# Kernel tuning notes

Hardware: AMD Instinct MI355X
Metric: run time of the kernel (lower is better)

The kernel has to match this reference:

```python
import jax, jax.numpy as jnp
import numpy as np

D_MODEL, EMB_DIM, ORDER, SEQ_LEN, BATCH = 768, 33, 64, 8192, 2


def setup_inputs() -> dict:
    key = jax.random.key(0)
    ks = jax.random.split(key, 9)
    x = jax.random.normal(ks[0], (BATCH, D_MODEL, SEQ_LEN), dtype=jnp.float32)

    # PositionalEmbedding: t in [0,1], complex exponential bands
    bands = (EMB_DIM - 1) // 2
    t = jnp.linspace(0.0, 1.0, SEQ_LEN, dtype=jnp.float32)[None, :, None]          # (1, L, 1)
    t_rescaled = jnp.linspace(0.0, SEQ_LEN - 1, SEQ_LEN, dtype=jnp.float32)[None, :, None]
    w_ang = 2.0 * jnp.pi * t_rescaled / SEQ_LEN                                     # (1, L, 1)
    f = jnp.linspace(1e-4, bands - 1, bands, dtype=jnp.float32)[None, None]         # (1, 1, bands)
    zc = jnp.exp(-1j * f.astype(jnp.complex64) * w_ang.astype(jnp.complex64))
    z = jnp.concatenate([t, zc.real, zc.imag], axis=-1)                             # (1, L, emb_dim)

    # Sin activation frequency (shared single instance across all MLP layers), w=1
    freq = jnp.ones((1, ORDER), dtype=jnp.float32)

    def lin(k, fan_out, fan_in):
        s = 1.0 / np.sqrt(fan_in)
        return jax.random.normal(k, (fan_out, fan_in), dtype=jnp.float32) * s

    W1 = lin(ks[1], ORDER, EMB_DIM)
    b1 = jax.random.normal(ks[2], (ORDER,), dtype=jnp.float32) * 0.02
    W2 = lin(ks[3], ORDER, ORDER)
    b2 = jax.random.normal(ks[4], (ORDER,), dtype=jnp.float32) * 0.02
    W3 = lin(ks[5], ORDER, ORDER)
    b3 = jax.random.normal(ks[6], (ORDER,), dtype=jnp.float32) * 0.02
    Wout = lin(ks[7], D_MODEL, ORDER)  # no bias

    # ExponentialModulation deltas (deterministic buffer)
    target, fast_pct, slow_pct = 0.01, 0.3, 1.5
    max_decay = np.log(target) / fast_pct
    min_decay = np.log(target) / slow_pct
    deltas = jnp.linspace(min_decay, max_decay, D_MODEL, dtype=jnp.float32)[None, None]  # (1,1,d)

    bias_D = jax.random.normal(ks[8], (D_MODEL,), dtype=jnp.float32)

    return {"x": x, "L": SEQ_LEN, "z": z, "t": t, "freq": freq,
            "W1": W1, "b1": b1, "W2": W2, "b2": b2, "W3": W3, "b3": b3,
            "Wout": Wout, "deltas": deltas, "bias_D": bias_D}


def reference(x, L, z, t, freq, W1, b1, W2, b2, W3, b3, Wout, deltas, bias_D):
    zL, tL = z[:, :L], t[:, :L]                      # (1, L, emb_dim), (1, L, 1)
    # Implicit filter MLP with shared Sin activation
    h = jnp.sin(freq * (jnp.einsum('ble,oe->blo', zL, W1) + b1))
    h = jnp.sin(freq * (jnp.einsum('blo,po->blp', h, W2) + b2))
    h = jnp.sin(freq * (jnp.einsum('blo,po->blp', h, W3) + b3))
    h = jnp.einsum('blo,do->bld', h, Wout)           # (1, L, d_model)
    # Exponential modulation
    h = h * jnp.exp(-tL * jnp.abs(deltas))
    k = h[0].T                                       # (d_model, L)
    # FFT-based long convolution (fftconv_ref with gelu=False).
    # torch: k_f = rfft(k, n)/n ; y = irfft(u_f*k_f, n, norm='forward') == standard irfft(u_f*rfft(k,n), n)
    fft_size = 2 * L
    k_f = jnp.fft.rfft(k, n=fft_size)                # (d_model, n//2+1) complex
    u_f = jnp.fft.rfft(x, n=fft_size)                # (B, d_model, n//2+1)
    y = jnp.fft.irfft(u_f * k_f, n=fft_size)[..., :L]
    out = y + x * bias_D[:, None]
    return out.astype(x.dtype)
```

## Files before the change

### kernel.cpp

```cpp
#include <hip/hip_runtime.h>
#include <hip/hip_fp16.h>
#include <math.h>

#define D_MODEL 768
#define EMB 33
#define ORDER 64
#define SEQ 8192
#define BATCH 2
#define M 8192

#define PI_F 3.14159265358979323846f

#define IDX(a) ((a) + ((a) >> 4) + ((a) >> 7))
#define LDS_SZ 8768

__device__ __forceinline__ int rev13(int x) { return (int)(__brev((unsigned)x) >> 19); }

__device__ __constant__ float C8[8] = {
    1.f, 0.9238795325f, 0.7071067812f, 0.3826834324f,
    0.f, -0.3826834324f, -0.7071067812f, -0.9238795325f };
__device__ __constant__ float S8n[8] = {
    0.f, -0.3826834324f, -0.7071067812f, -0.9238795325f,
    -1.f, -0.9238795325f, -0.7071067812f, -0.3826834324f };
__device__ __constant__ float S8p[8] = {
    0.f, 0.3826834324f, 0.7071067812f, 0.9238795325f,
    1.f, 0.9238795325f, 0.7071067812f, 0.3826834324f };

__global__ __launch_bounds__(256) void mlp_kernel(
    const float* __restrict__ z, const float* __restrict__ freq,
    const float* __restrict__ W1, const float* __restrict__ b1,
    const float* __restrict__ W2, const float* __restrict__ b2,
    const float* __restrict__ W3, const float* __restrict__ b3,
    float* __restrict__ h3T)
{
    __shared__ float zt[33 * 72];
    __shared__ float h1[64 * 72];
    __shared__ float h2[64 * 72];
    __shared__ float Wb[64 * 68];
    __shared__ float sfr[64], sb[64];
    int t = threadIdx.x;
    int l0 = blockIdx.x * 64;

    for (int i = t; i < 64 * 33; i += 256) {
        int l = i / 33, e = i - l * 33;
        zt[e * 72 + l] = z[(size_t)(l0 + l) * 33 + e];
    }
    for (int i = t; i < 64 * 33; i += 256) {
        int o = i / 33, e = i - o * 33;
        Wb[e * 68 + o] = W1[i];
    }
    if (t < 64) { sfr[t] = freq[t]; sb[t] = b1[t]; }
    __syncthreads();

    int lx = t & 15, oy = t >> 4;
    float fr4[4], bi4[4], acc[4][4];
#pragma unroll
    for (int i = 0; i < 4; ++i) { fr4[i] = sfr[4 * oy + i]; bi4[i] = sb[4 * oy + i]; }
#pragma unroll
    for (int c = 0; c < 4; ++c)
#pragma unroll
        for (int i = 0; i < 4; ++i) acc[c][i] = bi4[i];
    for (int e = 0; e < 33; ++e) {
        float4 hv = *(const float4*)&zt[e * 72 + 4 * lx];
        float4 wv = *(const float4*)&Wb[e * 68 + 4 * oy];
        float h[4] = {hv.x, hv.y, hv.z, hv.w}, w[4] = {wv.x, wv.y, wv.z, wv.w};
#pragma unroll
        for (int c = 0; c < 4; ++c)
#pragma unroll
            for (int i = 0; i < 4; ++i) acc[c][i] = fmaf(h[c], w[i], acc[c][i]);
    }
#pragma unroll
    for (int i = 0; i < 4; ++i) {
        float4 v = make_float4(__sinf(fr4[i] * acc[0][i]), __sinf(fr4[i] * acc[1][i]),
                               __sinf(fr4[i] * acc[2][i]), __sinf(fr4[i] * acc[3][i]));
        *(float4*)&h1[(4 * oy + i) * 72 + 4 * lx] = v;
    }
    __syncthreads();

    for (int i = t; i < 4096; i += 256) {
        int o = i >> 6, q = i & 63;
        Wb[q * 68 + o] = W2[i];
    }
    if (t < 64) sb[t] = b2[t];
    __syncthreads();
#pragma unroll
    for (int i = 0; i < 4; ++i) bi4[i] = sb[4 * oy + i];
#pragma unroll
    for (int c = 0; c < 4; ++c)
#pragma unroll
        for (int i = 0; i < 4; ++i) acc[c][i] = bi4[i];
    for (int q = 0; q < 64; ++q) {
        float4 hv = *(const float4*)&h1[q * 72 + 4 * lx];
        float4 wv = *(const float4*)&Wb[q * 68 + 4 * oy];
        float h[4] = {hv.x, hv.y, hv.z, hv.w}, w[4] = {wv.x, wv.y, wv.z, wv.w};
#pragma unroll
        for (int c = 0; c < 4; ++c)
#pragma unroll
            for (int i = 0; i < 4; ++i) acc[c][i] = fmaf(h[c], w[i], acc[c][i]);
    }
#pragma unroll
    for (int i = 0; i < 4; ++i) {
        float4 v = make_float4(__sinf(fr4[i] * acc[0][i]), __sinf(fr4[i] * acc[1][i]),
                               __sinf(fr4[i] * acc[2][i]), __sinf(fr4[i] * acc[3][i]));
        *(float4*)&h2[(4 * oy + i) * 72 + 4 * lx] = v;
    }
    __syncthreads();

    for (int i = t; i < 4096; i += 256) {
        int o = i >> 6, q = i & 63;
        Wb[q * 68 + o] = W3[i];
    }
    if (t < 64) sb[t] = b3[t];
    __syncthreads();
#pragma unroll
    for (int i = 0; i < 4; ++i) bi4[i] = sb[4 * oy + i];
#pragma unroll
    for (int c = 0; c < 4; ++c)
#pragma unroll
        for (int i = 0; i < 4; ++i) acc[c][i] = bi4[i];
    for (int q = 0; q < 64; ++q) {
        float4 hv = *(const float4*)&h2[q * 72 + 4 * lx];
        float4 wv = *(const float4*)&Wb[q * 68 + 4 * oy];
        float h[4] = {hv.x, hv.y, hv.z, hv.w}, w[4] = {wv.x, wv.y, wv.z, wv.w};
#pragma unroll
        for (int c = 0; c < 4; ++c)
#pragma unroll
            for (int i = 0; i < 4; ++i) acc[c][i] = fmaf(h[c], w[i], acc[c][i]);
    }
#pragma unroll
    for (int i = 0; i < 4; ++i) {
        float4 v = make_float4(__sinf(fr4[i] * acc[0][i]), __sinf(fr4[i] * acc[1][i]),
                               __sinf(fr4[i] * acc[2][i]), __sinf(fr4[i] * acc[3][i]));
        *(float4*)&h3T[(size_t)(4 * oy + i) * SEQ + l0 + 4 * lx] = v;
    }
}

__global__ __launch_bounds__(256) void filt_kernel(
    const float* __restrict__ h3T, const float* __restrict__ Wout,
    const float* __restrict__ tvec, const float* __restrict__ deltas,
    float* __restrict__ kout)
{
    __shared__ float ht[64 * 132];
    __shared__ float wt[64 * 68];
    int t = threadIdx.x;
    int l0 = blockIdx.x * 128, d0 = blockIdx.y * 64;

    for (int i = t; i < 64 * 128; i += 256) {
        int o = i >> 7, l = i & 127;
        ht[o * 132 + l] = h3T[(size_t)o * SEQ + l0 + l];
    }
    for (int i = t; i < 4096; i += 256) {
        int dd = i >> 6, kk = i & 63;
        wt[kk * 68 + dd] = Wout[(size_t)(d0 + dd) * 64 + kk];
    }
    __syncthreads();

    int lx = t & 31, dy = t >> 5;
    float acc[4][8];
#pragma unroll
    for (int c = 0; c < 4; ++c)
#pragma unroll
        for (int i = 0; i < 8; ++i) acc[c][i] = 0.f;
    for (int kk = 0; kk < 64; ++kk) {
        float4 hv = *(const float4*)&ht[kk * 132 + 4 * lx];
        float4 w0 = *(const float4*)&wt[kk * 68 + 8 * dy];
        float4 w1 = *(const float4*)&wt[kk * 68 + 8 * dy + 4];
        float h[4] = {hv.x, hv.y, hv.z, hv.w};
        float w[8] = {w0.x, w0.y, w0.z, w0.w, w1.x, w1.y, w1.z, w1.w};
#pragma unroll
        for (int c = 0; c < 4; ++c)
#pragma unroll
            for (int i = 0; i < 8; ++i) acc[c][i] = fmaf(h[c], w[i], acc[c][i]);
    }

    float4 tl4 = *(const float4*)&tvec[l0 + 4 * lx];
    float tl[4] = {tl4.x, tl4.y, tl4.z, tl4.w};
    float del[8];
#pragma unroll
    for (int i = 0; i < 8; ++i) del[i] = fabsf(deltas[d0 + 8 * dy + i]);
#pragma unroll
    for (int i = 0; i < 8; ++i) {
        int d = d0 + 8 * dy + i;
        float4 v = make_float4(acc[0][i] * __expf(-tl[0] * del[i]),
                               acc[1][i] * __expf(-tl[1] * del[i]),
                               acc[2][i] * __expf(-tl[2] * del[i]),
                               acc[3][i] * __expf(-tl[3] * del[i]));
        *(float4*)&kout[(size_t)d * SEQ + l0 + 4 * lx] = v;
    }
}

template<int H>
__device__ __forceinline__ void fwd8(float2* A, int t)
{
    constexpr int H4 = H / 4;
    int j0 = t & (H4 - 1);
    float c1, s1;
    __sincosf((-PI_F / (float)H) * (float)j0, &s1, &c1);
#pragma unroll
    for (int gg = 0; gg < 2; ++gg) {
        int g = t + (gg << 9);
        int j = g & (H4 - 1);
        int i = ((g & ~(H4 - 1)) << 3) | j;
        float c1g = c1, s1g = s1;
        if (H4 > 512 && gg == 1) {
            const float cR = 0.9238795325f, sR = -0.3826834324f;
            c1g = c1 * cR - s1 * sR;
            s1g = s1 * cR + c1 * sR;
        }
        float c2 = c1g * c1g - s1g * s1g, s2 = 2.f * c1g * s1g;
        float c3 = c2 * c2 - s2 * s2,     s3 = 2.f * c2 * s2;
        float xr[8], xi[8];
        int ad[8];
#pragma unroll
        for (int m = 0; m < 8; ++m) {
            ad[m] = IDX(i + m * H4);
            float2 v = A[ad[m]];
            xr[m] = v.x; xi[m] = v.y;
        }
        const float r = 0.70710678118f;
        float twc[4], tws[4];
        twc[0] = c1g;             tws[0] = s1g;
        twc[1] = r * (c1g + s1g); tws[1] = r * (s1g - c1g);
        twc[2] = s1g;             tws[2] = -c1g;
        twc[3] = r * (s1g - c1g); tws[3] = -r * (c1g + s1g);
#pragma unroll
        for (int m = 0; m < 4; ++m) {
            float ur = xr[m] + xr[m + 4], ui = xi[m] + xi[m + 4];
            float dr = xr[m] - xr[m + 4], di = xi[m] - xi[m + 4];
            xr[m] = ur; xi[m] = ui;
            xr[m + 4] = dr * twc[m] - di * tws[m];
            xi[m + 4] = dr * tws[m] + di * twc[m];
        }
#pragma unroll
        for (int base = 0; base < 8; base += 4)
#pragma unroll
            for (int mm = 0; mm < 2; ++mm) {
                int a = base + mm, b = a + 2;
                float ur = xr[a] + xr[b], ui = xi[a] + xi[b];
                float dr = xr[a] - xr[b], di = xi[a] - xi[b];
                xr[a] = ur; xi[a] = ui;
                if (mm == 0) { xr[b] = dr * c2 - di * s2; xi[b] = dr * s2 + di * c2; }
                else         { xr[b] = dr * s2 + di * c2; xi[b] = di * s2 - dr * c2; }
            }
#pragma unroll
        for (int m = 0; m < 8; m += 2) {
            float ur = xr[m] + xr[m + 1], ui = xi[m] + xi[m + 1];
            float dr = xr[m] - xr[m + 1], di = xi[m] - xi[m + 1];
            xr[m] = ur; xi[m] = ui;
            xr[m + 1] = dr * c3 - di * s3; xi[m + 1] = dr * s3 + di * c3;
        }
#pragma unroll
        for (int m = 0; m < 8; ++m) A[ad[m]] = make_float2(xr[m], xi[m]);
    }
}

template<int H>
__device__ __forceinline__ void inv8(float2* A, int t)
{
    int j0 = t & (H - 1);
    float ct, st;
    __sincosf((PI_F / (float)(4 * H)) * (float)j0, &st, &ct);
#pragma unroll
    for (int gg = 0; gg < 2; ++gg) {
        int g = t + (gg << 9);
        int j = g & (H - 1);
        int i = ((g & ~(H - 1)) << 3) | j;
        float c = ct, s = st;
        if (H > 512 && gg == 1) {
            const float cR = 0.9238795325f, sR = 0.3826834324f;
            c = ct * cR - st * sR;
            s = st * cR + ct * sR;
        }
        float c2 = c * c - s * s, s2 = 2.f * c * s;
        float c4 = c2 * c2 - s2 * s2, s4 = 2.f * c2 * s2;
        float xr[8], xi[8]; int ad[8];
#pragma unroll
        for (int m = 0; m < 8; ++m) {
            ad[m] = IDX(i + m * H);
            float2 v = A[ad[m]];
            xr[m] = v.x; xi[m] = v.y;
        }
#pragma unroll
        for (int m = 0; m < 8; m += 2) {
            float tr = xr[m + 1] * c4 - xi[m + 1] * s4;
            float ti = xr[m + 1] * s4 + xi[m + 1] * c4;
            xr[m + 1] = xr[m] - tr; xi[m + 1] = xi[m] - ti;
            xr[m]     = xr[m] + tr; xi[m]     = xi[m] + ti;
        }
#pragma unroll
        for (int base = 0; base < 8; base += 4)
#pragma unroll
            for (int mm = 0; mm < 2; ++mm) {
                int a = base + mm, b = a + 2;
                float tr, ti;
                if (mm == 0) { tr = xr[b] * c2 - xi[b] * s2; ti = xr[b] * s2 + xi[b] * c2; }
                else         { tr = -(xr[b] * s2 + xi[b] * c2); ti = xr[b] * c2 - xi[b] * s2; }
                xr[b] = xr[a] - tr; xi[b] = xi[a] - ti;
                xr[a] = xr[a] + tr; xi[a] = xi[a] + ti;
            }
        const float r = 0.70710678118f;
        float t3c[4], t3s[4];
        t3c[0] = c;           t3s[0] = s;
        t3c[1] = r * (c - s); t3s[1] = r * (c + s);
        t3c[2] = -s;          t3s[2] = c;
        t3c[3] = -r * (c + s); t3s[3] = r * (c - s);
#pragma unroll
        for (int m = 0; m < 4; ++m) {
            float tr = xr[m + 4] * t3c[m] - xi[m + 4] * t3s[m];
            float ti = xr[m + 4] * t3s[m] + xi[m + 4] * t3c[m];
            xr[m + 4] = xr[m] - tr; xi[m + 4] = xi[m] - ti;
            xr[m]     = xr[m] + tr; xi[m]     = xi[m] + ti;
        }
#pragma unroll
        for (int m = 0; m < 8; ++m) A[ad[m]] = make_float2(xr[m], xi[m]);
    }
}

__device__ __forceinline__ void fft_fwd(float2* A, int t)
{
    fwd8<4096>(A, t); __syncthreads();
    fwd8<512>(A, t);  __syncthreads();
    fwd8<64>(A, t);   __syncthreads();
    {
        int pb = IDX(16 * t);
        float fr[16], fi[16];
#pragma unroll
        for (int e = 0; e < 16; ++e) { float2 v = A[pb + e]; fr[e] = v.x; fi[e] = v.y; }
#pragma unroll
        for (int k = 0; k < 8; ++k) {
            float cs = C8[k], sn = S8n[k];
            float arr = fr[k], aii = fi[k], brr = fr[k + 8], bii = fi[k + 8];
            fr[k] = arr + brr; fi[k] = aii + bii;
            float dr = arr - brr, di = aii - bii;
            fr[k + 8] = dr * cs - di * sn; fi[k + 8] = dr * sn + di * cs;
        }
#pragma unroll
        for (int b0 = 0; b0 < 16; b0 += 8)
#pragma unroll
            for (int k = 0; k < 4; ++k) {
                float cs = C8[2 * k], sn = S8n[2 * k];
                int i0 = b0 + k, i1 = i0 + 4;
                float arr = fr[i0], aii = fi[i0], brr = fr[i1], bii = fi[i1];
                fr[i0] = arr + brr; fi[i0] = aii + bii;
                float dr = arr - brr, di = aii - bii;
                fr[i1] = dr * cs - di * sn; fi[i1] = dr * sn + di * cs;
            }
#pragma unroll
        for (int b0 = 0; b0 < 16; b0 += 4)
#pragma unroll
            for (int k = 0; k < 2; ++k) {
                float cs = C8[4 * k], sn = S8n[4 * k];
                int i0 = b0 + k, i1 = i0 + 2;
                float arr = fr[i0], aii = fi[i0], brr = fr[i1], bii = fi[i1];
                fr[i0] = arr + brr; fi[i0] = aii + bii;
                float dr = arr - brr, di = aii - bii;
                fr[i1] = dr * cs - di * sn; fi[i1] = dr * sn + di * cs;
            }
#pragma unroll
        for (int b0 = 0; b0 < 16; b0 += 2) {
            float arr = fr[b0], aii = fi[b0], brr = fr[b0 + 1], bii = fi[b0 + 1];
            fr[b0] = arr + brr; fi[b0] = aii + bii;
            fr[b0 + 1] = arr - brr; fi[b0 + 1] = aii - bii;
        }
#pragma unroll
        for (int e = 0; e < 16; ++e) A[pb + e] = make_float2(fr[e], fi[e]);
        __syncthreads();
    }
}

__device__ __forceinline__ void fft_inv(float2* A, int t)
{
    {
        int pb = IDX(16 * t);
        float fr[16], fi[16];
#pragma unroll
        for (int e = 0; e < 16; ++e) { float2 v = A[pb + e]; fr[e] = v.x; fi[e] = v.y; }
#pragma unroll
        for (int b0 = 0; b0 < 16; b0 += 2) {
            float arr = fr[b0], aii = fi[b0], brr = fr[b0 + 1], bii = fi[b0 + 1];
            fr[b0] = arr + brr; fi[b0] = aii + bii;
            fr[b0 + 1] = arr - brr; fi[b0 + 1] = aii - bii;
        }
#pragma unroll
        for (int b0 = 0; b0 < 16; b0 += 4)
#pragma unroll
            for (int k = 0; k < 2; ++k) {
                float cs = C8[4 * k], sn = S8p[4 * k];
                int i0 = b0 + k, i1 = i0 + 2;
                float arr = fr[i0], aii = fi[i0], brr = fr[i1], bii = fi[i1];
                float tr = brr * cs - bii * sn, ti = brr * sn + bii * cs;
                fr[i0] = arr + tr; fi[i0] = aii + ti;
                fr[i1] = arr - tr; fi[i1] = aii - ti;
            }
#pragma unroll
        for (int b0 = 0; b0 < 16; b0 += 8)
#pragma unroll
            for (int k = 0; k < 4; ++k) {
                float cs = C8[2 * k], sn = S8p[2 * k];
                int i0 = b0 + k, i1 = i0 + 4;
                float arr = fr[i0], aii = fi[i0], brr = fr[i1], bii = fi[i1];
                float tr = brr * cs - bii * sn, ti = brr * sn + bii * cs;
                fr[i0] = arr + tr; fi[i0] = aii + ti;
                fr[i1] = arr - tr; fi[i1] = aii - ti;
            }
#pragma unroll
        for (int k = 0; k < 8; ++k) {
            float cs = C8[k], sn = S8p[k];
            float arr = fr[k], aii = fi[k], brr = fr[k + 8], bii = fi[k + 8];
            float tr = brr * cs - bii * sn, ti = brr * sn + bii * cs;
            fr[k] = arr + tr; fi[k] = aii + ti;
            fr[k + 8] = arr - tr; fi[k + 8] = aii - ti;
        }
#pragma unroll
        for (int e = 0; e < 16; ++e) A[pb + e] = make_float2(fr[e], fi[e]);
        __syncthreads();
    }
    inv8<16>(A, t);   __syncthreads();
    inv8<128>(A, t);  __syncthreads();
    inv8<1024>(A, t); __syncthreads();
}

__global__ __launch_bounds__(512, 4) void kf_kernel(float* outk)
{
    __shared__ float2 A[LDS_SZ];
    int t = threadIdx.x, d = blockIdx.x;
    const float* kp = outk + (size_t)d * SEQ;
    for (int n = t; n < 4096; n += 512) {
        A[IDX(n)] = ((const float2*)kp)[n];
    }
    for (int n = 4096 + t; n < M; n += 512) A[IDX(n)] = make_float2(0.f, 0.f);
    __syncthreads();
    fft_fwd(A, t);

    __half2* P0 = (__half2*)(outk + (size_t)d * SEQ);
    __half2* P1 = (__half2*)(outk + (size_t)(D_MODEL + d) * SEQ);
    float cs, sn;
    __sincosf(-PI_F * (float)t * (1.0f / 8192.0f), &sn, &cs);
    const float cRo = 0.9807852804f, sRo = -0.1950903220f;
    for (int j = t; j <= 4096; j += 512) {
        int jm = (M - j) & (M - 1);
        int p0 = rev13(j), p1 = rev13(jm);
        float2 z1 = A[IDX(p0)], z2 = A[IDX(p1)];
        float Ar_ = 0.5f * (z1.x + z2.x), Ai_ = 0.5f * (z1.y - z2.y);
        float Br_ = 0.5f * (z1.y + z2.y), Bi_ = 0.5f * (z2.x - z1.x);
        float wbr = cs * Br_ - sn * Bi_, wbi = cs * Bi_ + sn * Br_;
        float K1r = Ar_ + wbr, K1i = Ai_ + wbi;
        float K2r = Ar_ - wbr, K2i = -(Ai_ - wbi);
        if (j == 0) {
            __half2 v = __floats2half2_rn(K1r, K2r);
            P0[0] = v; P1[0] = v;
        } else {
            __half2 v1 = __floats2half2_rn(K1r, K1i);
            P0[j] = v1; P1[j] = v1;
            if (j != 4096) {
                __half2 v2 = __floats2half2_rn(K2r, K2i);
                P0[M - j] = v2; P1[M - j] = v2;
            }
        }
        float cn = cs * cRo - sn * sRo; sn = sn * cRo + cs * sRo; cs = cn;
    }
}

__global__ __launch_bounds__(512, 4) void conv_kernel(
    const float* __restrict__ x, const float* __restrict__ bias,
    float* outk)
{
    __shared__ float2 A[LDS_SZ];
    int t = threadIdx.x, d = blockIdx.x, b = blockIdx.y;
    const float* xp = x + ((size_t)(b * D_MODEL + d)) * SEQ;
    float bd = bias[d];

#pragma unroll
    for (int idx = 0; idx < 8; ++idx) {
        int n = t + (idx << 9);
        A[IDX(n)] = ((const float2*)xp)[n];
    }
    for (int n = 4096 + t; n < M; n += 512) A[IDX(n)] = make_float2(0.f, 0.f);
    __syncthreads();
    fft_fwd(A, t);

    const __half2* P = (const __half2*)(outk + (size_t)(b * D_MODEL + d) * SEQ);
    float cs, sn;
    __sincosf(-PI_F * (float)t * (1.0f / 8192.0f), &sn, &cs);
    const float cRo = 0.9807852804f, sRo = -0.1950903220f;
    for (int j = t; j <= 4096; j += 512) {
        int jm = (M - j) & (M - 1);
        int p0 = rev13(j), p1 = rev13(jm);
        int q0 = IDX(p0), q1 = IDX(p1);
        float2 z1 = A[q0], z2 = A[q1];
        float Ar_ = 0.5f * (z1.x + z2.x), Ai_ = 0.5f * (z1.y - z2.y);
        float Br_ = 0.5f * (z1.y + z2.y), Bi_ = 0.5f * (z2.x - z1.x);
        float wbr = cs * Br_ - sn * Bi_, wbi = cs * Bi_ + sn * Br_;
        float U1r = Ar_ + wbr, U1i = Ai_ + wbi;
        float U2r = Ar_ - wbr, U2i = -(Ai_ - wbi);
        float K1r, K1i, K2r, K2i;
        if (j == 0) {
            __half2 v = P[0];
            K1r = __low2float(v) + bd;  K1i = 0.f;
            K2r = __high2float(v) + bd; K2i = 0.f;
        } else {
            __half2 v1 = P[j];
            __half2 v2 = P[M - j];
            K1r = __low2float(v1) + bd; K1i = __high2float(v1);
            K2r = __low2float(v2) + bd; K2i = __high2float(v2);
        }
        float P1r = U1r * K1r - U1i * K1i, P1i = U1r * K1i + U1i * K1r;
        float P2r = U2r * K2r - U2i * K2i, P2i = U2r * K2i + U2i * K2r;
        float Er = 0.5f * (P1r + P2r), Ei = 0.5f * (P1i - P2i);
        float Or = 0.5f * (P1r - P2r), Oi = 0.5f * (P1i + P2i);
        float G = cs * Oi - sn * Or;
        float H = cs * Or + sn * Oi;
        A[q0] = make_float2(Er - G, Ei + H);
        if (j != 0) A[q1] = make_float2(Er + G, -Ei + H);
        float cn = cs * cRo - sn * sRo; sn = sn * cRo + cs * sRo; cs = cn;
    }
    __syncthreads();
    fft_inv(A, t);

    const float invM = 1.0f / 8192.0f;
    float* op = outk + ((size_t)(b * D_MODEL + d)) * SEQ;
#pragma unroll
    for (int idx = 0; idx < 8; ++idx) {
        int n = t + (idx << 9);
        float2 v = A[IDX(n)];
        float2 ov;
        ov.x = v.x * invM;
        ov.y = v.y * invM;
        ((float2*)op)[n] = ov;
    }
}

extern "C" void kernel_launch(void* const* d_in, const int* in_sizes, int n_in,
                              void* d_out, int out_size, void* d_ws, size_t ws_size,
                              hipStream_t stream)
{
    (void)in_sizes; (void)n_in; (void)out_size; (void)d_ws; (void)ws_size;
    const float* x      = (const float*)d_in[0];
    const float* z      = (const float*)d_in[2];
    const float* tvec   = (const float*)d_in[3];
    const float* freq   = (const float*)d_in[4];
    const float* W1     = (const float*)d_in[5];
    const float* b1     = (const float*)d_in[6];
    const float* W2     = (const float*)d_in[7];
    const float* b2     = (const float*)d_in[8];
    const float* W3     = (const float*)d_in[9];
    const float* b3     = (const float*)d_in[10];
    const float* Wout   = (const float*)d_in[11];
    const float* deltas = (const float*)d_in[12];
    const float* bias   = (const float*)d_in[13];
    float* out = (float*)d_out;

    float* h3T = out + ((size_t)(2 * D_MODEL - 64) * SEQ);
    float* k   = out;

    hipLaunchKernelGGL(mlp_kernel, dim3(SEQ / 64), dim3(256), 0, stream,
                       z, freq, W1, b1, W2, b2, W3, b3, h3T);
    hipLaunchKernelGGL(filt_kernel, dim3(SEQ / 128, D_MODEL / 64), dim3(256), 0, stream,
                       h3T, Wout, tvec, deltas, k);
    hipLaunchKernelGGL(kf_kernel, dim3(D_MODEL), dim3(512), 0, stream, out);
    hipLaunchKernelGGL(conv_kernel, dim3(D_MODEL, BATCH), dim3(512), 0, stream,
                       x, bias, out);
}
```

Before: 234.1 us.

## Exploit zero padding: split FFT into two half-size transforms with twiddle pre/post

Replaces the full 8192-point complex FFT over a half-zero-padded signal with a first radix-2 stage done analytically at load time. Each input sample is written twice, once plain and once multiplied by a twiddle, so the remaining work is two independent 4096-point FFTs. The inverse is recombined with a twiddle at the store. Blocks now use 1024 threads that each do one radix-8 group per stage, with a radix-8 final stage instead of radix-16. This removes the redundant butterflies on the zero half and the per-thread loop over two groups, at the cost of more threads per block and extra sincos calls in the load and store loops.

```diff
diff --git a/kernel.cpp b/kernel.cpp
--- a/kernel.cpp
+++ b/kernel.cpp
@@ -189,181 +189,149 @@
     }
 }
 
+
+template<int H8>
+__device__ __forceinline__ void fwd8g(float2* A, int t)
+{
+    constexpr int H4 = H8 / 4;
+    int j = t & (H4 - 1);
+    int i = ((t & ~(H4 - 1)) << 3) | j;
+    float c1, s1;
+    __sincosf((-PI_F / (float)H8) * (float)j, &s1, &c1);
+    float c2 = c1 * c1 - s1 * s1, s2 = 2.f * c1 * s1;
+    float c3 = c2 * c2 - s2 * s2, s3 = 2.f * c2 * s2;
+    float xr[8], xi[8];
+    int ad[8];
+#pragma unroll
+    for (int m = 0; m < 8; ++m) {
+        ad[m] = IDX(i + m * H4);
+        float2 v = A[ad[m]];
+        xr[m] = v.x; xi[m] = v.y;
+    }
+    const float r = 0.70710678118f;
+    float twc[4], tws[4];
+    twc[0] = c1;            tws[0] = s1;
+    twc[1] = r * (c1 + s1); tws[1] = r * (s1 - c1);
+    twc[2] = s1;            tws[2] = -c1;
+    twc[3] = r * (s1 - c1); tws[3] = -r * (c1 + s1);
+#pragma unroll
+    for (int m = 0; m < 4; ++m) {
+        float ur = xr[m] + xr[m + 4], ui = xi[m] + xi[m + 4];
+        float dr = xr[m] - xr[m + 4], di = xi[m] - xi[m + 4];
+        xr[m] = ur; xi[m] = ui;
+        xr[m + 4] = dr * twc[m] - di * tws[m];
+        xi[m + 4] = dr * tws[m] + di * twc[m];
+    }
+#pragma unroll
+    for (int base = 0; base < 8; base += 4)
+#pragma unroll
+        for (int mm = 0; mm < 2; ++mm) {
+            int a = base + mm, b = a + 2;
+            float ur = xr[a] + xr[b], ui = xi[a] + xi[b];
+            float dr = xr[a] - xr[b], di = xi[a] - xi[b];
+            xr[a] = ur; xi[a] = ui;
+            if (mm == 0) { xr[b] = dr * c2 - di * s2; xi[b] = dr * s2 + di * c2; }
+            else         { xr[b] = dr * s2 + di * c2; xi[b] = di * s2 - dr * c2; }
+        }
+#pragma unroll
+    for (int m = 0; m < 8; m += 2) {
+        float ur = xr[m] + xr[m + 1], ui = xi[m] + xi[m + 1];
+        float dr = xr[m] - xr[m + 1], di = xi[m] - xi[m + 1];
+        xr[m] = ur; xi[m] = ui;
+        xr[m + 1] = dr * c3 - di * s3; xi[m + 1] = dr * s3 + di * c3;
+    }
+#pragma unroll
+    for (int m = 0; m < 8; ++m) A[ad[m]] = make_float2(xr[m], xi[m]);
+}
+
 template<int H>
-__device__ __forceinline__ void fwd8(float2* A, int t)
-{
-    constexpr int H4 = H / 4;
-    int j0 = t & (H4 - 1);
-    float c1, s1;
-    __sincosf((-PI_F / (float)H) * (float)j0, &s1, &c1);
-#pragma unroll
-    for (int gg = 0; gg < 2; ++gg) {
-        int g = t + (gg << 9);
-        int j = g & (H4 - 1);
-        int i = ((g & ~(H4 - 1)) << 3) | j;
-        float c1g = c1, s1g = s1;
-        if (H4 > 512 && gg == 1) {
-            const float cR = 0.9238795325f, sR = -0.3826834324f;
-            c1g = c1 * cR - s1 * sR;
-            s1g = s1 * cR + c1 * sR;
-        }
-        float c2 = c1g * c1g - s1g * s1g, s2 = 2.f * c1g * s1g;
-        float c3 = c2 * c2 - s2 * s2,     s3 = 2.f * c2 * s2;
-        float xr[8], xi[8];
-        int ad[8];
-#pragma unroll
-        for (int m = 0; m < 8; ++m) {
-            ad[m] = IDX(i + m * H4);
-            float2 v = A[ad[m]];
-            xr[m] = v.x; xi[m] = v.y;
-        }
-        const float r = 0.70710678118f;
-        float twc[4], tws[4];
-        twc[0] = c1g;             tws[0] = s1g;
-        twc[1] = r * (c1g + s1g); tws[1] = r * (s1g - c1g);
-        twc[2] = s1g;             tws[2] = -c1g;
-        twc[3] = r * (s1g - c1g); tws[3] = -r * (c1g + s1g);
-#pragma unroll
-        for (int m = 0; m < 4; ++m) {
-            float ur = xr[m] + xr[m + 4], ui = xi[m] + xi[m + 4];
-            float dr = xr[m] - xr[m + 4], di = xi[m] - xi[m + 4];
-            xr[m] = ur; xi[m] = ui;
-            xr[m + 4] = dr * twc[m] - di * tws[m];
-            xi[m + 4] = dr * tws[m] + di * twc[m];
-        }
-#pragma unroll
-        for (int base = 0; base < 8; base += 4)
-#pragma unroll
-            for (int mm = 0; mm < 2; ++mm) {
-                int a = base + mm, b = a + 2;
-                float ur = xr[a] + xr[b], ui = xi[a] + xi[b];
-                float dr = xr[a] - xr[b], di = xi[a] - xi[b];
-                xr[a] = ur; xi[a] = ui;
-                if (mm == 0) { xr[b] = dr * c2 - di * s2; xi[b] = dr * s2 + di * c2; }
-                else         { xr[b] = dr * s2 + di * c2; xi[b] = di * s2 - dr * c2; }
-            }
-#pragma unroll
-        for (int m = 0; m < 8; m += 2) {
-            float ur = xr[m] + xr[m + 1], ui = xi[m] + xi[m + 1];
-            float dr = xr[m] - xr[m + 1], di = xi[m] - xi[m + 1];
-            xr[m] = ur; xi[m] = ui;
-            xr[m + 1] = dr * c3 - di * s3; xi[m + 1] = dr * s3 + di * c3;
-        }
-#pragma unroll
-        for (int m = 0; m < 8; ++m) A[ad[m]] = make_float2(xr[m], xi[m]);
-    }
-}
-
-template<int H>
-__device__ __forceinline__ void inv8(float2* A, int t)
-{
-    int j0 = t & (H - 1);
-    float ct, st;
-    __sincosf((PI_F / (float)(4 * H)) * (float)j0, &st, &ct);
-#pragma unroll
-    for (int gg = 0; gg < 2; ++gg) {
-        int g = t + (gg << 9);
-        int j = g & (H - 1);
-        int i = ((g & ~(H - 1)) << 3) | j;
-        float c = ct, s = st;
-        if (H > 512 && gg == 1) {
-            const float cR = 0.9238795325f, sR = 0.3826834324f;
-            c = ct * cR - st * sR;
-            s = st * cR + ct * sR;
-        }
-        float c2 = c * c - s * s, s2 = 2.f * c * s;
-        float c4 = c2 * c2 - s2 * s2, s4 = 2.f * c2 * s2;
-        float xr[8], xi[8]; int ad[8];
-#pragma unroll
-        for (int m = 0; m < 8; ++m) {
-            ad[m] = IDX(i + m * H);
-            float2 v = A[ad[m]];
-            xr[m] = v.x; xi[m] = v.y;
-        }
-#pragma unroll
-        for (int m = 0; m < 8; m += 2) {
-            float tr = xr[m + 1] * c4 - xi[m + 1] * s4;
-            float ti = xr[m + 1] * s4 + xi[m + 1] * c4;
-            xr[m + 1] = xr[m] - tr; xi[m + 1] = xi[m] - ti;
-            xr[m]     = xr[m] + tr; xi[m]     = xi[m] + ti;
-        }
-#pragma unroll
-        for (int base = 0; base < 8; base += 4)
-#pragma unroll
-            for (int mm = 0; mm < 2; ++mm) {
-                int a = base + mm, b = a + 2;
-                float tr, ti;
-                if (mm == 0) { tr = xr[b] * c2 - xi[b] * s2; ti = xr[b] * s2 + xi[b] * c2; }
-                else         { tr = -(xr[b] * s2 + xi[b] * c2); ti = xr[b] * c2 - xi[b] * s2; }
-                xr[b] = xr[a] - tr; xi[b] = xi[a] - ti;
-                xr[a] = xr[a] + tr; xi[a] = xi[a] + ti;
-            }
-        const float r = 0.70710678118f;
-        float t3c[4], t3s[4];
-        t3c[0] = c;           t3s[0] = s;
-        t3c[1] = r * (c - s); t3s[1] = r * (c + s);
-        t3c[2] = -s;          t3s[2] = c;
-        t3c[3] = -r * (c + s); t3s[3] = r * (c - s);
-#pragma unroll
-        for (int m = 0; m < 4; ++m) {
-            float tr = xr[m + 4] * t3c[m] - xi[m + 4] * t3s[m];
-            float ti = xr[m + 4] * t3s[m] + xi[m + 4] * t3c[m];
-            xr[m + 4] = xr[m] - tr; xi[m + 4] = xi[m] - ti;
-            xr[m]     = xr[m] + tr; xi[m]     = xi[m] + ti;
-        }
-#pragma unroll
-        for (int m = 0; m < 8; ++m) A[ad[m]] = make_float2(xr[m], xi[m]);
-    }
+__device__ __forceinline__ void inv8g(float2* A, int t)
+{
+    int j = t & (H - 1);
+    int i = ((t & ~(H - 1)) << 3) | j;
+    float c, s;
+    __sincosf((PI_F / (float)(4 * H)) * (float)j, &s, &c);
+    float c2 = c * c - s * s, s2 = 2.f * c * s;
+    float c4 = c2 * c2 - s2 * s2, s4 = 2.f * c2 * s2;
+    float xr[8], xi[8]; int ad[8];
+#pragma unroll
+    for (int m = 0; m < 8; ++m) {
+        ad[m] = IDX(i + m * H);
+        float2 v = A[ad[m]];
+        xr[m] = v.x; xi[m] = v.y;
+    }
+#pragma unroll
+    for (int m = 0; m < 8; m += 2) {
+        float tr = xr[m + 1] * c4 - xi[m + 1] * s4;
+        float ti = xr[m + 1] * s4 + xi[m + 1] * c4;
+        xr[m + 1] = xr[m] - tr; xi[m + 1] = xi[m] - ti;
+        xr[m]     = xr[m] + tr; xi[m]     = xi[m] + ti;
+    }
+#pragma unroll
+    for (int base = 0; base < 8; base += 4)
+#pragma unroll
+        for (int mm = 0; mm < 2; ++mm) {
+            int a = base + mm, b = a + 2;
+            float tr, ti;
+            if (mm == 0) { tr = xr[b] * c2 - xi[b] * s2; ti = xr[b] * s2 + xi[b] * c2; }
+            else         { tr = -(xr[b] * s2 + xi[b] * c2); ti = xr[b] * c2 - xi[b] * s2; }
+            xr[b] = xr[a] - tr; xi[b] = xi[a] - ti;
+            xr[a] = xr[a] + tr; xi[a] = xi[a] + ti;
+        }
+    const float r = 0.70710678118f;
+    float t3c[4], t3s[4];
+    t3c[0] = c;            t3s[0] = s;
+    t3c[1] = r * (c - s);  t3s[1] = r * (c + s);
+    t3c[2] = -s;           t3s[2] = c;
+    t3c[3] = -r * (c + s); t3s[3] = r * (c - s);
+#pragma unroll
+    for (int m = 0; m < 4; ++m) {
+        float tr = xr[m + 4] * t3c[m] - xi[m + 4] * t3s[m];
+        float ti = xr[m + 4] * t3s[m] + xi[m + 4] * t3c[m];
+        xr[m + 4] = xr[m] - tr; xi[m + 4] = xi[m] - ti;
+        xr[m]     = xr[m] + tr; xi[m]     = xi[m] + ti;
+    }
+#pragma unroll
+    for (int m = 0; m < 8; ++m) A[ad[m]] = make_float2(xr[m], xi[m]);
 }
 
 __device__ __forceinline__ void fft_fwd(float2* A, int t)
 {
-    fwd8<4096>(A, t); __syncthreads();
-    fwd8<512>(A, t);  __syncthreads();
-    fwd8<64>(A, t);   __syncthreads();
+    fwd8g<2048>(A, t); __syncthreads();
+    fwd8g<256>(A, t);  __syncthreads();
+    fwd8g<32>(A, t);   __syncthreads();
     {
-        int pb = IDX(16 * t);
-        float fr[16], fi[16];
-#pragma unroll
-        for (int e = 0; e < 16; ++e) { float2 v = A[pb + e]; fr[e] = v.x; fi[e] = v.y; }
-#pragma unroll
-        for (int k = 0; k < 8; ++k) {
-            float cs = C8[k], sn = S8n[k];
-            float arr = fr[k], aii = fi[k], brr = fr[k + 8], bii = fi[k + 8];
-            fr[k] = arr + brr; fi[k] = aii + bii;
-            float dr = arr - brr, di = aii - bii;
-            fr[k + 8] = dr * cs - di * sn; fi[k + 8] = dr * sn + di * cs;
-        }
-#pragma unroll
-        for (int b0 = 0; b0 < 16; b0 += 8)
-#pragma unroll
-            for (int k = 0; k < 4; ++k) {
-                float cs = C8[2 * k], sn = S8n[2 * k];
-                int i0 = b0 + k, i1 = i0 + 4;
-                float arr = fr[i0], aii = fi[i0], brr = fr[i1], bii = fi[i1];
-                fr[i0] = arr + brr; fi[i0] = aii + bii;
-                float dr = arr - brr, di = aii - bii;
-                fr[i1] = dr * cs - di * sn; fi[i1] = dr * sn + di * cs;
-            }
-#pragma unroll
-        for (int b0 = 0; b0 < 16; b0 += 4)
+        int pb = IDX(8 * t);
+        float fr[8], fi[8];
+#pragma unroll
+        for (int e = 0; e < 8; ++e) { float2 v = A[pb + e]; fr[e] = v.x; fi[e] = v.y; }
+#pragma unroll
+        for (int k = 0; k < 4; ++k) {
+            float cs = C8[2 * k], sn = S8n[2 * k];
+            float ar = fr[k], ai = fi[k], br = fr[k + 4], bi = fi[k + 4];
+            fr[k] = ar + br; fi[k] = ai + bi;
+            float dr = ar - br, di = ai - bi;
+            fr[k + 4] = dr * cs - di * sn; fi[k + 4] = dr * sn + di * cs;
+        }
+#pragma unroll
+        for (int b0 = 0; b0 < 8; b0 += 4)
 #pragma unroll
             for (int k = 0; k < 2; ++k) {
                 float cs = C8[4 * k], sn = S8n[4 * k];
                 int i0 = b0 + k, i1 = i0 + 2;
-                float arr = fr[i0], aii = fi[i0], brr = fr[i1], bii = fi[i1];
-                fr[i0] = arr + brr; fi[i0] = aii + bii;
-                float dr = arr - brr, di = aii - bii;
+                float ar = fr[i0], ai = fi[i0], br = fr[i1], bi = fi[i1];
+                fr[i0] = ar + br; fi[i0] = ai + bi;
+                float dr = ar - br, di = ai - bi;
                 fr[i1] = dr * cs - di * sn; fi[i1] = dr * sn + di * cs;
             }
 #pragma unroll
-        for (int b0 = 0; b0 < 16; b0 += 2) {
-            float arr = fr[b0], aii = fi[b0], brr = fr[b0 + 1], bii = fi[b0 + 1];
-            fr[b0] = arr + brr; fi[b0] = aii + bii;
-            fr[b0 + 1] = arr - brr; fi[b0 + 1] = aii - bii;
-        }
-#pragma unroll
-        for (int e = 0; e < 16; ++e) A[pb + e] = make_float2(fr[e], fi[e]);
+        for (int b0 = 0; b0 < 8; b0 += 2) {
+            float ar = fr[b0], ai = fi[b0], br = fr[b0 + 1], bi = fi[b0 + 1];
+            fr[b0] = ar + br; fi[b0] = ai + bi;
+            fr[b0 + 1] = ar - br; fi[b0 + 1] = ai - bi;
+        }
+#pragma unroll
+        for (int e = 0; e < 8; ++e) A[pb + e] = make_float2(fr[e], fi[e]);
         __syncthreads();
     }
 }
@@ -371,64 +339,58 @@
 __device__ __forceinline__ void fft_inv(float2* A, int t)
 {
     {
-        int pb = IDX(16 * t);
-        float fr[16], fi[16];
-#pragma unroll
-        for (int e = 0; e < 16; ++e) { float2 v = A[pb + e]; fr[e] = v.x; fi[e] = v.y; }
-#pragma unroll
-        for (int b0 = 0; b0 < 16; b0 += 2) {
-            float arr = fr[b0], aii = fi[b0], brr = fr[b0 + 1], bii = fi[b0 + 1];
-            fr[b0] = arr + brr; fi[b0] = aii + bii;
-            fr[b0 + 1] = arr - brr; fi[b0 + 1] = aii - bii;
-        }
-#pragma unroll
-        for (int b0 = 0; b0 < 16; b0 += 4)
+        int pb = IDX(8 * t);
+        float fr[8], fi[8];
+#pragma unroll
+        for (int e = 0; e < 8; ++e) { float2 v = A[pb + e]; fr[e] = v.x; fi[e] = v.y; }
+#pragma unroll
+        for (int b0 = 0; b0 < 8; b0 += 2) {
+            float ar = fr[b0], ai = fi[b0], br = fr[b0 + 1], bi = fi[b0 + 1];
+            fr[b0] = ar + br; fi[b0] = ai + bi;
+            fr[b0 + 1] = ar - br; fi[b0 + 1] = ai - bi;
+        }
+#pragma unroll
+        for (int b0 = 0; b0 < 8; b0 += 4)
 #pragma unroll
             for (int k = 0; k < 2; ++k) {
                 float cs = C8[4 * k], sn = S8p[4 * k];
                 int i0 = b0 + k, i1 = i0 + 2;
-                float arr = fr[i0], aii = fi[i0], brr = fr[i1], bii = fi[i1];
-                float tr = brr * cs - bii * sn, ti = brr * sn + bii * cs;
-                fr[i0] = arr + tr; fi[i0] = aii + ti;
-                fr[i1] = arr - tr; fi[i1] = aii - ti;
+                float ar = fr[i0], ai = fi[i0], br = fr[i1], bi = fi[i1];
+                float tr = br * cs - bi * sn, ti = br * sn + bi * cs;
+                fr[i0] = ar + tr; fi[i0] = ai + ti;
+                fr[i1] = ar - tr; fi[i1] = ai - ti;
             }
 #pragma unroll
-        for (int b0 = 0; b0 < 16; b0 += 8)
-#pragma unroll
-            for (int k = 0; k < 4; ++k) {
-                float cs = C8[2 * k], sn = S8p[2 * k];
-                int i0 = b0 + k, i1 = i0 + 4;
-                float arr = fr[i0], aii = fi[i0], brr = fr[i1], bii = fi[i1];
-                float tr = brr * cs - bii * sn, ti = brr * sn + bii * cs;
-                fr[i0] = arr + tr; fi[i0] = aii + ti;
-                fr[i1] = arr - tr; fi[i1] = aii - ti;
-            }
-#pragma unroll
-        for (int k = 0; k < 8; ++k) {
-            float cs = C8[k], sn = S8p[k];
-            float arr = fr[k], aii = fi[k], brr = fr[k + 8], bii = fi[k + 8];
-            float tr = brr * cs - bii * sn, ti = brr * sn + bii * cs;
-            fr[k] = arr + tr; fi[k] = aii + ti;
-            fr[k + 8] = arr - tr; fi[k + 8] = aii - ti;
-        }
-#pragma unroll
-        for (int e = 0; e < 16; ++e) A[pb + e] = make_float2(fr[e], fi[e]);
+        for (int k = 0; k < 4; ++k) {
+            float cs = C8[2 * k], sn = S8p[2 * k];
+            float ar = fr[k], ai = fi[k], br = fr[k + 4], bi = fi[k + 4];
+            float tr = br * cs - bi * sn, ti = br * sn + bi * cs;
+            fr[k] = ar + tr; fi[k] = ai + ti;
+            fr[k + 4] = ar - tr; fi[k + 4] = ai - ti;
+        }
+#pragma unroll
+        for (int e = 0; e < 8; ++e) A[pb + e] = make_float2(fr[e], fi[e]);
         __syncthreads();
     }
-    inv8<16>(A, t);   __syncthreads();
-    inv8<128>(A, t);  __syncthreads();
-    inv8<1024>(A, t); __syncthreads();
-}
-
-__global__ __launch_bounds__(512, 4) void kf_kernel(float* outk)
+    inv8g<8>(A, t);   __syncthreads();
+    inv8g<64>(A, t);  __syncthreads();
+    inv8g<512>(A, t); __syncthreads();
+}
+
+__global__ __launch_bounds__(1024, 8) void kf_kernel(float* outk)
 {
     __shared__ float2 A[LDS_SZ];
     int t = threadIdx.x, d = blockIdx.x;
     const float* kp = outk + (size_t)d * SEQ;
-    for (int n = t; n < 4096; n += 512) {
-        A[IDX(n)] = ((const float2*)kp)[n];
-    }
-    for (int n = 4096 + t; n < M; n += 512) A[IDX(n)] = make_float2(0.f, 0.f);
+#pragma unroll
+    for (int idx = 0; idx < 4; ++idx) {
+        int n = t + (idx << 10);
+        float2 v = ((const float2*)kp)[n];
+        A[IDX(n)] = v;
+        float c, s;
+        __sincosf((-PI_F / 4096.0f) * (float)n, &s, &c);
+        A[IDX(n + 4096)] = make_float2(v.x * c - v.y * s, v.x * s + v.y * c);
+    }
     __syncthreads();
     fft_fwd(A, t);
 
@@ -436,8 +398,8 @@
     __half2* P1 = (__half2*)(outk + (size_t)(D_MODEL + d) * SEQ);
     float cs, sn;
     __sincosf(-PI_F * (float)t * (1.0f / 8192.0f), &sn, &cs);
-    const float cRo = 0.9807852804f, sRo = -0.1950903220f;
-    for (int j = t; j <= 4096; j += 512) {
+    const float cRo = 0.9238795325f, sRo = -0.3826834324f;
+    for (int j = t; j <= 4096; j += 1024) {
         int jm = (M - j) & (M - 1);
         int p0 = rev13(j), p1 = rev13(jm);
         float2 z1 = A[IDX(p0)], z2 = A[IDX(p1)];
@@ -461,7 +423,7 @@
     }
 }
 
-__global__ __launch_bounds__(512, 4) void conv_kernel(
+__global__ __launch_bounds__(1024, 8) void conv_kernel(
     const float* __restrict__ x, const float* __restrict__ bias,
     float* outk)
 {
@@ -471,19 +433,22 @@
     float bd = bias[d];
 
 #pragma unroll
-    for (int idx = 0; idx < 8; ++idx) {
-        int n = t + (idx << 9);
-        A[IDX(n)] = ((const float2*)xp)[n];
-    }
-    for (int n = 4096 + t; n < M; n += 512) A[IDX(n)] = make_float2(0.f, 0.f);
+    for (int idx = 0; idx < 4; ++idx) {
+        int n = t + (idx << 10);
+        float2 v = ((const float2*)xp)[n];
+        A[IDX(n)] = v;
+        float c, s;
+        __sincosf((-PI_F / 4096.0f) * (float)n, &s, &c);
+        A[IDX(n + 4096)] = make_float2(v.x * c - v.y * s, v.x * s + v.y * c);
+    }
     __syncthreads();
     fft_fwd(A, t);
 
     const __half2* P = (const __half2*)(outk + (size_t)(b * D_MODEL + d) * SEQ);
     float cs, sn;
     __sincosf(-PI_F * (float)t * (1.0f / 8192.0f), &sn, &cs);
-    const float cRo = 0.9807852804f, sRo = -0.1950903220f;
-    for (int j = t; j <= 4096; j += 512) {
+    const float cRo = 0.9238795325f, sRo = -0.3826834324f;
+    for (int j = t; j <= 4096; j += 1024) {
         int jm = (M - j) & (M - 1);
         int p0 = rev13(j), p1 = rev13(jm);
         int q0 = IDX(p0), q1 = IDX(p1);
@@ -520,12 +485,15 @@
     const float invM = 1.0f / 8192.0f;
     float* op = outk + ((size_t)(b * D_MODEL + d)) * SEQ;
 #pragma unroll
-    for (int idx = 0; idx < 8; ++idx) {
-        int n = t + (idx << 9);
-        float2 v = A[IDX(n)];
+    for (int idx = 0; idx < 4; ++idx) {
+        int n = t + (idx << 10);
+        float2 a = A[IDX(n)], bb = A[IDX(n + 4096)];
+        float c, s;
+        __sincosf((PI_F / 4096.0f) * (float)n, &s, &c);
+        float tr = bb.x * c - bb.y * s, ti = bb.x * s + bb.y * c;
         float2 ov;
-        ov.x = v.x * invM;
-        ov.y = v.y * invM;
+        ov.x = (a.x + tr) * invM;
+        ov.y = (a.y + ti) * invM;
         ((float2*)op)[n] = ov;
     }
 }
@@ -557,7 +525,7 @@
                        z, freq, W1, b1, W2, b2, W3, b3, h3T);
     hipLaunchKernelGGL(filt_kernel, dim3(SEQ / 128, D_MODEL / 64), dim3(256), 0, stream,
                        h3T, Wout, tvec, deltas, k);
-    hipLaunchKernelGGL(kf_kernel, dim3(D_MODEL), dim3(512), 0, stream, out);
-    hipLaunchKernelGGL(conv_kernel, dim3(D_MODEL, BATCH), dim3(512), 0, stream,
+    hipLaunchKernelGGL(kf_kernel, dim3(D_MODEL), dim3(1024), 0, stream, out);
+    hipLaunchKernelGGL(conv_kernel, dim3(D_MODEL, BATCH), dim3(1024), 0, stream,
                        x, bias, out);
 }
```

Result: slower. 278.7 us (+19.0%).

## Fold zero-padding radix-2 stage into load and store, shrink FFT to halves

Applied to the files above, without the earlier changes.

The forward FFT now handles the zero-padded half analytically. At load time each input is written twice: once as-is and once multiplied by a twiddle, which performs the first decimation-in-frequency stage. What remains is two independent 4096-point transforms, with the register radix-16 pass split into two radix-8 passes and smaller strides in the LDS stages. The inverse mirrors this: the final radix-2 combine is applied only to the first L outputs during the store. This removes a butterfly stage's worth of arithmetic and the zero-fill writes, at the cost of an extra sincos per element on load and store.

```diff
diff --git a/kernel.cpp b/kernel.cpp
--- a/kernel.cpp
+++ b/kernel.cpp
@@ -318,49 +318,43 @@
 
 __device__ __forceinline__ void fft_fwd(float2* A, int t)
 {
-    fwd8<4096>(A, t); __syncthreads();
-    fwd8<512>(A, t);  __syncthreads();
-    fwd8<64>(A, t);   __syncthreads();
+    fwd8<2048>(A, t); __syncthreads();
+    fwd8<256>(A, t);  __syncthreads();
+    fwd8<32>(A, t);   __syncthreads();
     {
         int pb = IDX(16 * t);
         float fr[16], fi[16];
 #pragma unroll
         for (int e = 0; e < 16; ++e) { float2 v = A[pb + e]; fr[e] = v.x; fi[e] = v.y; }
 #pragma unroll
-        for (int k = 0; k < 8; ++k) {
-            float cs = C8[k], sn = S8n[k];
-            float arr = fr[k], aii = fi[k], brr = fr[k + 8], bii = fi[k + 8];
-            fr[k] = arr + brr; fi[k] = aii + bii;
-            float dr = arr - brr, di = aii - bii;
-            fr[k + 8] = dr * cs - di * sn; fi[k + 8] = dr * sn + di * cs;
-        }
-#pragma unroll
-        for (int b0 = 0; b0 < 16; b0 += 8)
+        for (int bb = 0; bb < 16; bb += 8) {
 #pragma unroll
             for (int k = 0; k < 4; ++k) {
                 float cs = C8[2 * k], sn = S8n[2 * k];
-                int i0 = b0 + k, i1 = i0 + 4;
-                float arr = fr[i0], aii = fi[i0], brr = fr[i1], bii = fi[i1];
-                fr[i0] = arr + brr; fi[i0] = aii + bii;
-                float dr = arr - brr, di = aii - bii;
+                int i0 = bb + k, i1 = i0 + 4;
+                float ar = fr[i0], ai = fi[i0], br = fr[i1], bi = fi[i1];
+                fr[i0] = ar + br; fi[i0] = ai + bi;
+                float dr = ar - br, di = ai - bi;
                 fr[i1] = dr * cs - di * sn; fi[i1] = dr * sn + di * cs;
             }
 #pragma unroll
-        for (int b0 = 0; b0 < 16; b0 += 4)
-#pragma unroll
-            for (int k = 0; k < 2; ++k) {
-                float cs = C8[4 * k], sn = S8n[4 * k];
-                int i0 = b0 + k, i1 = i0 + 2;
-                float arr = fr[i0], aii = fi[i0], brr = fr[i1], bii = fi[i1];
-                fr[i0] = arr + brr; fi[i0] = aii + bii;
-                float dr = arr - brr, di = aii - bii;
-                fr[i1] = dr * cs - di * sn; fi[i1] = dr * sn + di * cs;
-            }
-#pragma unroll
-        for (int b0 = 0; b0 < 16; b0 += 2) {
-            float arr = fr[b0], aii = fi[b0], brr = fr[b0 + 1], bii = fi[b0 + 1];
-            fr[b0] = arr + brr; fi[b0] = aii + bii;
-            fr[b0 + 1] = arr - brr; fi[b0 + 1] = aii - bii;
+            for (int b0 = 0; b0 < 8; b0 += 4)
+#pragma unroll
+                for (int k = 0; k < 2; ++k) {
+                    float cs = C8[4 * k], sn = S8n[4 * k];
+                    int i0 = bb + b0 + k, i1 = i0 + 2;
+                    float ar = fr[i0], ai = fi[i0], br = fr[i1], bi = fi[i1];
+                    fr[i0] = ar + br; fi[i0] = ai + bi;
+                    float dr = ar - br, di = ai - bi;
+                    fr[i1] = dr * cs - di * sn; fi[i1] = dr * sn + di * cs;
+                }
+#pragma unroll
+            for (int b0 = 0; b0 < 8; b0 += 2) {
+                int i0 = bb + b0;
+                float ar = fr[i0], ai = fi[i0], br = fr[i0 + 1], bi = fi[i0 + 1];
+                fr[i0] = ar + br; fi[i0] = ai + bi;
+                fr[i0 + 1] = ar - br; fi[i0 + 1] = ai - bi;
+            }
         }
 #pragma unroll
         for (int e = 0; e < 16; ++e) A[pb + e] = make_float2(fr[e], fi[e]);
@@ -376,48 +370,42 @@
 #pragma unroll
         for (int e = 0; e < 16; ++e) { float2 v = A[pb + e]; fr[e] = v.x; fi[e] = v.y; }
 #pragma unroll
-        for (int b0 = 0; b0 < 16; b0 += 2) {
-            float arr = fr[b0], aii = fi[b0], brr = fr[b0 + 1], bii = fi[b0 + 1];
-            fr[b0] = arr + brr; fi[b0] = aii + bii;
-            fr[b0 + 1] = arr - brr; fi[b0 + 1] = aii - bii;
-        }
-#pragma unroll
-        for (int b0 = 0; b0 < 16; b0 += 4)
-#pragma unroll
-            for (int k = 0; k < 2; ++k) {
-                float cs = C8[4 * k], sn = S8p[4 * k];
-                int i0 = b0 + k, i1 = i0 + 2;
-                float arr = fr[i0], aii = fi[i0], brr = fr[i1], bii = fi[i1];
-                float tr = brr * cs - bii * sn, ti = brr * sn + bii * cs;
-                fr[i0] = arr + tr; fi[i0] = aii + ti;
-                fr[i1] = arr - tr; fi[i1] = aii - ti;
-            }
-#pragma unroll
-        for (int b0 = 0; b0 < 16; b0 += 8)
+        for (int bb = 0; bb < 16; bb += 8) {
+#pragma unroll
+            for (int b0 = 0; b0 < 8; b0 += 2) {
+                int i0 = bb + b0;
+                float ar = fr[i0], ai = fi[i0], br = fr[i0 + 1], bi = fi[i0 + 1];
+                fr[i0] = ar + br; fi[i0] = ai + bi;
+                fr[i0 + 1] = ar - br; fi[i0 + 1] = ai - bi;
+            }
+#pragma unroll
+            for (int b0 = 0; b0 < 8; b0 += 4)
+#pragma unroll
+                for (int k = 0; k < 2; ++k) {
+                    float cs = C8[4 * k], sn = S8p[4 * k];
+                    int i0 = bb + b0 + k, i1 = i0 + 2;
+                    float ar = fr[i0], ai = fi[i0], br = fr[i1], bi = fi[i1];
+                    float tr = br * cs - bi * sn, ti = br * sn + bi * cs;
+                    fr[i0] = ar + tr; fi[i0] = ai + ti;
+                    fr[i1] = ar - tr; fi[i1] = ai - ti;
+                }
 #pragma unroll
             for (int k = 0; k < 4; ++k) {
                 float cs = C8[2 * k], sn = S8p[2 * k];
-                int i0 = b0 + k, i1 = i0 + 4;
-                float arr = fr[i0], aii = fi[i0], brr = fr[i1], bii = fi[i1];
-                float tr = brr * cs - bii * sn, ti = brr * sn + bii * cs;
-                fr[i0] = arr + tr; fi[i0] = aii + ti;
-                fr[i1] = arr - tr; fi[i1] = aii - ti;
-            }
-#pragma unroll
-        for (int k = 0; k < 8; ++k) {
-            float cs = C8[k], sn = S8p[k];
-            float arr = fr[k], aii = fi[k], brr = fr[k + 8], bii = fi[k + 8];
-            float tr = brr * cs - bii * sn, ti = brr * sn + bii * cs;
-            fr[k] = arr + tr; fi[k] = aii + ti;
-            fr[k + 8] = arr - tr; fi[k + 8] = aii - ti;
+                int i0 = bb + k, i1 = i0 + 4;
+                float ar = fr[i0], ai = fi[i0], br = fr[i1], bi = fi[i1];
+                float tr = br * cs - bi * sn, ti = br * sn + bi * cs;
+                fr[i0] = ar + tr; fi[i0] = ai + ti;
+                fr[i1] = ar - tr; fi[i1] = ai - ti;
+            }
         }
 #pragma unroll
         for (int e = 0; e < 16; ++e) A[pb + e] = make_float2(fr[e], fi[e]);
         __syncthreads();
     }
-    inv8<16>(A, t);   __syncthreads();
-    inv8<128>(A, t);  __syncthreads();
-    inv8<1024>(A, t); __syncthreads();
+    inv8<8>(A, t);   __syncthreads();
+    inv8<64>(A, t);  __syncthreads();
+    inv8<512>(A, t); __syncthreads();
 }
 
 __global__ __launch_bounds__(512, 4) void kf_kernel(float* outk)
@@ -425,10 +413,15 @@
     __shared__ float2 A[LDS_SZ];
     int t = threadIdx.x, d = blockIdx.x;
     const float* kp = outk + (size_t)d * SEQ;
-    for (int n = t; n < 4096; n += 512) {
-        A[IDX(n)] = ((const float2*)kp)[n];
-    }
-    for (int n = 4096 + t; n < M; n += 512) A[IDX(n)] = make_float2(0.f, 0.f);
+#pragma unroll
+    for (int idx = 0; idx < 8; ++idx) {
+        int n = t + (idx << 9);
+        float2 v = ((const float2*)kp)[n];
+        A[IDX(n)] = v;
+        float c, s;
+        __sincosf((-PI_F / 4096.0f) * (float)n, &s, &c);
+        A[IDX(n + 4096)] = make_float2(v.x * c - v.y * s, v.x * s + v.y * c);
+    }
     __syncthreads();
     fft_fwd(A, t);
 
@@ -473,9 +466,12 @@
 #pragma unroll
     for (int idx = 0; idx < 8; ++idx) {
         int n = t + (idx << 9);
-        A[IDX(n)] = ((const float2*)xp)[n];
-    }
-    for (int n = 4096 + t; n < M; n += 512) A[IDX(n)] = make_float2(0.f, 0.f);
+        float2 v = ((const float2*)xp)[n];
+        A[IDX(n)] = v;
+        float c, s;
+        __sincosf((-PI_F / 4096.0f) * (float)n, &s, &c);
+        A[IDX(n + 4096)] = make_float2(v.x * c - v.y * s, v.x * s + v.y * c);
+    }
     __syncthreads();
     fft_fwd(A, t);
 
@@ -522,10 +518,13 @@
 #pragma unroll
     for (int idx = 0; idx < 8; ++idx) {
         int n = t + (idx << 9);
-        float2 v = A[IDX(n)];
+        float2 a = A[IDX(n)], bb = A[IDX(n + 4096)];
+        float c, s;
+        __sincosf((PI_F / 4096.0f) * (float)n, &s, &c);
+        float tr = bb.x * c - bb.y * s, ti = bb.x * s + bb.y * c;
         float2 ov;
-        ov.x = v.x * invM;
-        ov.y = v.y * invM;
+        ov.x = (a.x + tr) * invM;
+        ov.y = (a.y + ti) * invM;
         ((float2*)op)[n] = ov;
     }
 }
```

Result: slower. 247.8 us (+5.8%).
